# Optimization experiments

Hardware: AMD Instinct MI355X
Metric: run time of the kernel (lower is better)

## Reference

```python
import jax, jax.numpy as jnp
import numpy as np
from jax.ops import segment_sum

N_NODES = 10000
N_EDGES = 320000


def leaky_relu(x):
    return jnp.where(x >= 0, x, 0.01 * x)


def gcn_layer(edge_h, src, dst, W, b):
    # (1) node h = mean of incoming edge features
    deg = segment_sum(jnp.ones((edge_h.shape[0],), edge_h.dtype), dst, num_segments=N_NODES)
    deg = jnp.maximum(deg, 1.0)
    h = segment_sum(edge_h, dst, num_segments=N_NODES) / deg[:, None]
    # (2) update_all: node h = sum over in-edges of src node h
    h2 = segment_sum(h[src], dst, num_segments=N_NODES)
    # (3) edge h = mean of endpoint node features
    eh = 0.5 * (h2[src] + h2[dst])
    # (4) linear on edge features
    return eh @ W.T + b


def setup_inputs() -> dict:
    key = jax.random.key(0)
    ks = jax.random.split(key, 20)
    d_in, d_h, d_out = 128, 256, 64
    inp = {
        'inputs1': jax.random.normal(ks[0], (N_EDGES, d_in), jnp.float32),
        'src1': jax.random.randint(ks[1], (N_EDGES,), 0, N_NODES, jnp.int32),
        'dst1': jax.random.randint(ks[2], (N_EDGES,), 0, N_NODES, jnp.int32),
        'inputs2': jax.random.normal(ks[3], (N_EDGES, d_in), jnp.float32),
        'src2': jax.random.randint(ks[4], (N_EDGES,), 0, N_NODES, jnp.int32),
        'dst2': jax.random.randint(ks[5], (N_EDGES,), 0, N_NODES, jnp.int32),
        'W11': jax.random.normal(ks[6], (d_h, d_in), jnp.float32) * 0.05,
        'b11': jax.random.normal(ks[7], (d_h,), jnp.float32) * 0.05,
        'W12': jax.random.normal(ks[8], (d_h, d_h), jnp.float32) * 0.05,
        'b12': jax.random.normal(ks[9], (d_h,), jnp.float32) * 0.05,
        'W21': jax.random.normal(ks[10], (d_h, d_in), jnp.float32) * 0.05,
        'b21': jax.random.normal(ks[11], (d_h,), jnp.float32) * 0.05,
        'W22': jax.random.normal(ks[12], (d_h, d_h), jnp.float32) * 0.05,
        'b22': jax.random.normal(ks[13], (d_h,), jnp.float32) * 0.05,
        'W3': jax.random.normal(ks[14], (d_out, 2 * d_h), jnp.float32) * 0.05,
        'b3': jax.random.normal(ks[15], (d_out,), jnp.float32) * 0.05,
    }
    return inp


def reference(inputs1, src1, dst1, inputs2, src2, dst2,
              W11, b11, W12, b12, W21, b21, W22, b22, W3, b3):
    h1 = leaky_relu(gcn_layer(inputs1, src1, dst1, W11, b11))
    h1 = leaky_relu(gcn_layer(h1, src1, dst1, W12, b12))
    h1 = jnp.mean(h1, axis=0)
    h2 = leaky_relu(gcn_layer(inputs2, src2, dst2, W21, b21))
    h2 = leaky_relu(gcn_layer(h2, src2, dst2, W22, b22))
    h2 = jnp.mean(h2, axis=0)
    out = jnp.concatenate((h1, h2), axis=0)
    return out @ W3.T + b3
```

## Files before the change

### kernel.cpp

```cpp
#include <hip/hip_runtime.h>
#include <cstddef>

#define NN 10000

typedef unsigned int u32;
typedef unsigned short u16;
typedef __attribute__((ext_vector_type(8))) short short8;
typedef __attribute__((ext_vector_type(4))) float f32x4;

__device__ __forceinline__ float lrelu(float x) { return x >= 0.f ? x : 0.01f * x; }

__device__ __forceinline__ float bf_lo(u32 v) { union { u32 i; float f; } c; c.i = v << 16; return c.f; }
__device__ __forceinline__ float bf_hi(u32 v) { union { u32 i; float f; } c; c.i = v & 0xFFFF0000u; return c.f; }
__device__ __forceinline__ u32 rne_bits(float f) {
  union { float f; u32 i; } c; c.f = f;
  return c.i + 0x7FFFu + ((c.i >> 16) & 1u);
}
__device__ __forceinline__ u32 pack2(float a, float b) {
  return (rne_bits(a) >> 16) | (rne_bits(b) & 0xFFFF0000u);
}

__global__ __launch_bounds__(256) void wconv_kernel(
    const float* __restrict__ a, const float* __restrict__ b,
    const float* __restrict__ c, const float* __restrict__ d,
    u16* __restrict__ oa, u16* __restrict__ ob,
    u16* __restrict__ oc, u16* __restrict__ od,
    int* __restrict__ degbase ) {
  int i = blockIdx.x * 256 + threadIdx.x;
  if (i < 32768) oa[i] = (u16)(rne_bits(a[i]) >> 16);
  else if (i < 98304) ob[i - 32768] = (u16)(rne_bits(b[i - 32768]) >> 16);
  else if (i < 131072) oc[i - 98304] = (u16)(rne_bits(c[i - 98304]) >> 16);
  else if (i < 196608) od[i - 131072] = (u16)(rne_bits(d[i - 131072]) >> 16);
  if (i < 4 * NN) degbase[i] = 0;
}

__global__ __launch_bounds__(256) void count_b_kernel(const int* __restrict__ dstA,
// ... 16 lines not shown
  __shared__ int wsum[16];
  __shared__ int wpre[16];
  __shared__ int carry_s;
  const int tid = threadIdx.x;
  const int lane = tid & 63, w = tid >> 6;
  if (tid == 0) carry_s = 0;
  __syncthreads();
  for (int base = 0; base < n; base += 1024) {
    int i = base + tid;
    int x = (i < n) ? degi[i] : 0;
    int v = x;
#pragma unroll
    for (int d = 1; d < 64; d <<= 1) {
      int t = __shfl_up(v, d);
      if (lane >= d) v += t;
    }
    if (lane == 63) wsum[w] = v;
    __syncthreads();
    if (tid == 0) {
      int s = carry_s;
#pragma unroll
      for (int j = 0; j < 16; ++j) { int t = wsum[j]; wpre[j] = s; s += t; }
      carry_s = s;
    }
    __syncthreads();
    if (i < n) {
      off[i] = wpre[w] + (v - x);
      rdeg[i] = 1.0f / fmaxf((float)x, 1.0f);
    }
    __syncthreads();
  }
}

__global__ __launch_bounds__(256) void fill_b_kernel(const int* __restrict__ srcA,
                                                     const int* __restrict__ dstA,
                                                     const int* __restrict__ srcB,
                                                     const int* __restrict__ dstB,
                                                     const int* __restrict__ offbase,
                                                     int* __restrict__ degbase,
                                                     int* __restrict__ eid_sb,
                                                     int* __restrict__ esrc_sb, int E) {
  const int g = blockIdx.y;
  const int* src = g ? srcB : srcA;
  const int* dst = g ? dstB : dstA;
  const int* off = offbase + (size_t)g * NN;
  int* cursor = degbase + (size_t)g * 2 * NN + NN;
  int* eid_s = eid_sb + (size_t)g * E;
  int* esrc_s = esrc_sb + (size_t)g * E;
  int e = blockIdx.x * 256 + threadIdx.x;
  if (e < E) {
    int d = dst[e];
    int p = off[d] + atomicAdd(&cursor[d], 1);
    eid_s[p] = e;
    esrc_s[p] = src[e];
  }
}

__global__ __launch_bounds__(256) void gatherA_b_kernel(
    const float* __restrict__ featA, const float* __restrict__ featB,
    const int* __restrict__ gidxb, const int* __restrict__ offbase,
    const int* __restrict__ degbase, const float* __restrict__ rdegbase,
    u32* __restrict__ outbfb , int E) {
  const int g = blockIdx.y;
  const float* feat = g ? featB : featA;
  const int* gidx = gidxb + (size_t)g * E;
  const int* off = offbase + (size_t)g * NN;
  const int* degi = degbase + (size_t)g * 2 * NN;
  const float* rdeg = rdegbase + (size_t)g * NN;
  u32* outbf = outbfb + (size_t)g * NN * 64;
  const int n = (blockIdx.x << 2) + (threadIdx.x >> 6);
  const int lane = threadIdx.x & 63;
  const int hl = lane & 31, h = lane >> 5;
  const int o = off[n], d = degi[n];
  const int fo = hl << 2;
  float4 acc = make_float4(0.f, 0.f, 0.f, 0.f);
  for (int c0 = 0; c0 < d; c0 += 64) {
    const int m = min(64, d - c0);
    const int gg = (lane < m) ? gidx[o + c0 + lane] : 0;
    const int pairs = m >> 1;
    int i = 0;
    for (; i + 4 <= pairs; i += 4) {
      const int e0 = 2 * i + h;
      const int s0 = __shfl(gg, e0), s1 = __shfl(gg, e0 + 2);
      const int s2 = __shfl(gg, e0 + 4), s3 = __shfl(gg, e0 + 6);
      const float4 v0 = *(const float4*)&feat[(s0 << 7) + fo];
      const float4 v1 = *(const float4*)&feat[(s1 << 7) + fo];
      const float4 v2 = *(const float4*)&feat[(s2 << 7) + fo];
      const float4 v3 = *(const float4*)&feat[(s3 << 7) + fo];
      acc.x += (v0.x + v1.x) + (v2.x + v3.x);
      acc.y += (v0.y + v1.y) + (v2.y + v3.y);
      acc.z += (v0.z + v1.z) + (v2.z + v3.z);
      acc.w += (v0.w + v1.w) + (v2.w + v3.w);
    }
    for (; i < pairs; ++i) {
      const int s0 = __shfl(gg, 2 * i + h);
      const float4 v0 = *(const float4*)&feat[(s0 << 7) + fo];
      acc.x += v0.x; acc.y += v0.y; acc.z += v0.z; acc.w += v0.w;
    }
    if (m & 1) {
      const int s0 = __shfl(gg, m - 1);
      const float wgt = (h == 0) ? 1.f : 0.f;
      const float4 v0 = *(const float4*)&feat[(s0 << 7) + fo];
      acc.x = fmaf(v0.x, wgt, acc.x);
      acc.y = fmaf(v0.y, wgt, acc.y);
      acc.z = fmaf(v0.z, wgt, acc.z);
      acc.w = fmaf(v0.w, wgt, acc.w);
    }
  }
  acc.x += __shfl(acc.x, lane ^ 32);
  acc.y += __shfl(acc.y, lane ^ 32);
  acc.z += __shfl(acc.z, lane ^ 32);
  acc.w += __shfl(acc.w, lane ^ 32);
  if (h == 0) {
    const float sc = rdeg[n];
    uint2 r;
    r.x = pack2(acc.x * sc, acc.y * sc);
    r.y = pack2(acc.z * sc, acc.w * sc);
    *(uint2*)&outbf[(size_t)n * 64 + (hl << 1)] = r;
  }
}

__global__ __launch_bounds__(256) void gatherB_b_kernel(
    const u32* __restrict__ featb , const int* __restrict__ gidxb,
    const int* __restrict__ offbase, const int* __restrict__ degbase,
    u32* __restrict__ outbfb, int E) {
  const int g = blockIdx.y;
  const u32* feat = featb + (size_t)g * NN * 64;
  const int* gidx = gidxb + (size_t)g * E;
  const int* off = offbase + (size_t)g * NN;
  const int* degi = degbase + (size_t)g * 2 * NN;
  u32* outbf = outbfb + (size_t)g * NN * 64;
  const int n = (blockIdx.x << 2) + (threadIdx.x >> 6);
  const int lane = threadIdx.x & 63;
  const int hl = lane & 31, h = lane >> 5;
  const int o = off[n], d = degi[n];
  const int fo = hl << 1;
  float4 acc = make_float4(0.f, 0.f, 0.f, 0.f);
  for (int c0 = 0; c0 < d; c0 += 64) {
    const int m = min(64, d - c0);
    const int gg = (lane < m) ? gidx[o + c0 + lane] : 0;
    const int pairs = m >> 1;
    int i = 0;
    for (; i + 4 <= pairs; i += 4) {
      const int e0 = 2 * i + h;
      const int s0 = __shfl(gg, e0), s1 = __shfl(gg, e0 + 2);
      const int s2 = __shfl(gg, e0 + 4), s3 = __shfl(gg, e0 + 6);
      const uint2 v0 = *(const uint2*)&feat[(s0 << 6) + fo];
      const uint2 v1 = *(const uint2*)&feat[(s1 << 6) + fo];
      const uint2 v2 = *(const uint2*)&feat[(s2 << 6) + fo];
      const uint2 v3 = *(const uint2*)&feat[(s3 << 6) + fo];
      acc.x += (bf_lo(v0.x) + bf_lo(v1.x)) + (bf_lo(v2.x) + bf_lo(v3.x));
      acc.y += (bf_hi(v0.x) + bf_hi(v1.x)) + (bf_hi(v2.x) + bf_hi(v3.x));
      acc.z += (bf_lo(v0.y) + bf_lo(v1.y)) + (bf_lo(v2.y) + bf_lo(v3.y));
      acc.w += (bf_hi(v0.y) + bf_hi(v1.y)) + (bf_hi(v2.y) + bf_hi(v3.y));
    }
    for (; i < pairs; ++i) {
      const int s0 = __shfl(gg, 2 * i + h);
      const uint2 v0 = *(const uint2*)&feat[(s0 << 6) + fo];
      acc.x += bf_lo(v0.x); acc.y += bf_hi(v0.x);
      acc.z += bf_lo(v0.y); acc.w += bf_hi(v0.y);
    }
    if (m & 1) {
      const int s0 = __shfl(gg, m - 1);
      const float wgt = (h == 0) ? 1.f : 0.f;
      const uint2 v0 = *(const uint2*)&feat[(s0 << 6) + fo];
      acc.x = fmaf(bf_lo(v0.x), wgt, acc.x);
      acc.y = fmaf(bf_hi(v0.x), wgt, acc.y);
      acc.z = fmaf(bf_lo(v0.y), wgt, acc.z);
      acc.w = fmaf(bf_hi(v0.y), wgt, acc.w);
    }
  }
  acc.x += __shfl(acc.x, lane ^ 32);
  acc.y += __shfl(acc.y, lane ^ 32);
  acc.z += __shfl(acc.z, lane ^ 32);
  acc.w += __shfl(acc.w, lane ^ 32);
  if (h == 0) {
    uint2 r;
    r.x = pack2(acc.x, acc.y);
    r.y = pack2(acc.z, acc.w);
    *(uint2*)&outbf[(size_t)n * 64 + (hl << 1)] = r;
  }
}

__device__ __forceinline__ void acc_bf8n(float4& aL, float4& aH, uint4 v,
                                         const float4& znL, const float4& znH,
                                         const float4& bL, const float4& bH) {
  aL.x += lrelu(0.5f * (bf_lo(v.x) + znL.x) + bL.x);
  aL.y += lrelu(0.5f * (bf_hi(v.x) + znL.y) + bL.y);
  aL.z += lrelu(0.5f * (bf_lo(v.y) + znL.z) + bL.z);
  aL.w += lrelu(0.5f * (bf_hi(v.y) + znL.w) + bL.w);
  aH.x += lrelu(0.5f * (bf_lo(v.z) + znH.x) + bH.x);
  aH.y += lrelu(0.5f * (bf_hi(v.z) + znH.y) + bH.y);
  aH.z += lrelu(0.5f * (bf_lo(v.w) + znH.z) + bH.z);
  aH.w += lrelu(0.5f * (bf_hi(v.w) + znH.w) + bH.w);
}
__device__ __forceinline__ void acc_bf8w(float4& aL, float4& aH, uint4 v,
                                         const float4& znL, const float4& znH,
                                         const float4& bL, const float4& bH, float wgt) {
  aL.x += wgt * lrelu(0.5f * (bf_lo(v.x) + znL.x) + bL.x);
  aL.y += wgt * lrelu(0.5f * (bf_hi(v.x) + znL.y) + bL.y);
  aL.z += wgt * lrelu(0.5f * (bf_lo(v.y) + znL.z) + bL.z);
  aL.w += wgt * lrelu(0.5f * (bf_hi(v.y) + znL.w) + bL.w);
  aH.x += wgt * lrelu(0.5f * (bf_lo(v.z) + znH.x) + bH.x);
  aH.y += wgt * lrelu(0.5f * (bf_hi(v.z) + znH.y) + bH.y);
  aH.z += wgt * lrelu(0.5f * (bf_lo(v.w) + znH.z) + bH.z);
  aH.w += wgt * lrelu(0.5f * (bf_hi(v.w) + znH.w) + bH.w);
}

__global__ __launch_bounds__(256) void passC_b_kernel(
    const u32* __restrict__ Zb_, const int* __restrict__ esrcb,
    const int* __restrict__ offbase, const int* __restrict__ degbase,
    const float* __restrict__ rdegbase,
    const float* __restrict__ biasA, const float* __restrict__ biasB,
    u32* __restrict__ hBb, int E) {
  const int g = blockIdx.y;
  const u32* Z = Zb_ + (size_t)g * NN * 128;
  const int* esrc = esrcb + (size_t)g * E;
  const int* off = offbase + (size_t)g * NN;
  const int* degi = degbase + (size_t)g * 2 * NN;
  const float* rdeg = rdegbase + (size_t)g * NN;
  const float* bias = g ? biasB : biasA;
  u32* hB = hBb + (size_t)g * NN * 128;
  const int n = (blockIdx.x << 2) + (threadIdx.x >> 6);
  const int lane = threadIdx.x & 63;
  const int hl = lane & 31, h = lane >> 5;
  const int o = off[n], d = degi[n];
  const int fo = hl << 2;
  const uint4 znv = *(const uint4*)&Z[(n << 7) + fo];
  const float4 znL = make_float4(bf_lo(znv.x), bf_hi(znv.x), bf_lo(znv.y), bf_hi(znv.y));
  const float4 znH = make_float4(bf_lo(znv.z), bf_hi(znv.z), bf_lo(znv.w), bf_hi(znv.w));
  const float4 bL = *(const float4*)&bias[hl << 3];
  const float4 bH = *(const float4*)&bias[(hl << 3) + 4];
  float4 aL = make_float4(0.f, 0.f, 0.f, 0.f), aH = make_float4(0.f, 0.f, 0.f, 0.f);
  for (int c0 = 0; c0 < d; c0 += 64) {
    const int m = min(64, d - c0);
    const int gg = (lane < m) ? esrc[o + c0 + lane] : 0;
    const int pairs = m >> 1;
    int i = 0;
    for (; i + 4 <= pairs; i += 4) {
      const int e0 = 2 * i + h;
      const int s0 = __shfl(gg, e0), s1 = __shfl(gg, e0 + 2);
      const int s2 = __shfl(gg, e0 + 4), s3 = __shfl(gg, e0 + 6);
      const uint4 z0 = *(const uint4*)&Z[(s0 << 7) + fo];
      const uint4 z1 = *(const uint4*)&Z[(s1 << 7) + fo];
      const uint4 z2 = *(const uint4*)&Z[(s2 << 7) + fo];
      const uint4 z3 = *(const uint4*)&Z[(s3 << 7) + fo];
      acc_bf8n(aL, aH, z0, znL, znH, bL, bH);
      acc_bf8n(aL, aH, z1, znL, znH, bL, bH);
      acc_bf8n(aL, aH, z2, znL, znH, bL, bH);
      acc_bf8n(aL, aH, z3, znL, znH, bL, bH);
    }
    for (; i < pairs; ++i) {
      const int s0 = __shfl(gg, 2 * i + h);
      const uint4 z0 = *(const uint4*)&Z[(s0 << 7) + fo];
      acc_bf8n(aL, aH, z0, znL, znH, bL, bH);
    }
    if (m & 1) {
      const int s0 = __shfl(gg, m - 1);
      const float wgt = (h == 0) ? 1.f : 0.f;
      const uint4 z0 = *(const uint4*)&Z[(s0 << 7) + fo];
      acc_bf8w(aL, aH, z0, znL, znH, bL, bH, wgt);
    }
  }
  aL.x += __shfl(aL.x, lane ^ 32); aL.y += __shfl(aL.y, lane ^ 32);
  aL.z += __shfl(aL.z, lane ^ 32); aL.w += __shfl(aL.w, lane ^ 32);
  aH.x += __shfl(aH.x, lane ^ 32); aH.y += __shfl(aH.y, lane ^ 32);
  aH.z += __shfl(aH.z, lane ^ 32); aH.w += __shfl(aH.w, lane ^ 32);
  if (h == 0) {
    const float r = rdeg[n];
    uint4 outv;
    outv.x = pack2(aL.x * r, aL.y * r);
    outv.y = pack2(aL.z * r, aL.w * r);
    outv.z = pack2(aH.x * r, aH.y * r);
    outv.w = pack2(aH.z * r, aH.w * r);
    *(uint4*)&hB[(n << 7) + fo] = outv;
  }
}

__global__ __launch_bounds__(256) void gatherC_b_kernel(
    const u32* __restrict__ featb , const int* __restrict__ gidxb,
    const int* __restrict__ offbase, const int* __restrict__ degbase,
    u32* __restrict__ outbfb, int E) {
  const int g = blockIdx.y;
  const u32* feat = featb + (size_t)g * NN * 128;
  const int* gidx = gidxb + (size_t)g * E;
  const int* off = offbase + (size_t)g * NN;
  const int* degi = degbase + (size_t)g * 2 * NN;
  u32* outbf = outbfb + (size_t)g * NN * 128;
  const int n = (blockIdx.x << 2) + (threadIdx.x >> 6);
  const int lane = threadIdx.x & 63;
  const int hl = lane & 31, h = lane >> 5;
  const int o = off[n], d = degi[n];
  const int fo = hl << 2;
  float4 aL = make_float4(0.f, 0.f, 0.f, 0.f), aH = make_float4(0.f, 0.f, 0.f, 0.f);
  for (int c0 = 0; c0 < d; c0 += 64) {
    const int m = min(64, d - c0);
    const int gg = (lane < m) ? gidx[o + c0 + lane] : 0;
    const int pairs = m >> 1;
    int i = 0;
    for (; i + 4 <= pairs; i += 4) {
      const int e0 = 2 * i + h;
      const int s0 = __shfl(gg, e0), s1 = __shfl(gg, e0 + 2);
      const int s2 = __shfl(gg, e0 + 4), s3 = __shfl(gg, e0 + 6);
      const uint4 z0 = *(const uint4*)&feat[(s0 << 7) + fo];
      const uint4 z1 = *(const uint4*)&feat[(s1 << 7) + fo];
      const uint4 z2 = *(const uint4*)&feat[(s2 << 7) + fo];
      const uint4 z3 = *(const uint4*)&feat[(s3 << 7) + fo];
      aL.x += (bf_lo(z0.x) + bf_lo(z1.x)) + (bf_lo(z2.x) + bf_lo(z3.x));
      aL.y += (bf_hi(z0.x) + bf_hi(z1.x)) + (bf_hi(z2.x) + bf_hi(z3.x));
      aL.z += (bf_lo(z0.y) + bf_lo(z1.y)) + (bf_lo(z2.y) + bf_lo(z3.y));
      aL.w += (bf_hi(z0.y) + bf_hi(z1.y)) + (bf_hi(z2.y) + bf_hi(z3.y));
      aH.x += (bf_lo(z0.z) + bf_lo(z1.z)) + (bf_lo(z2.z) + bf_lo(z3.z));
      aH.y += (bf_hi(z0.z) + bf_hi(z1.z)) + (bf_hi(z2.z) + bf_hi(z3.z));
      aH.z += (bf_lo(z0.w) + bf_lo(z1.w)) + (bf_lo(z2.w) + bf_lo(z3.w));
      aH.w += (bf_hi(z0.w) + bf_hi(z1.w)) + (bf_hi(z2.w) + bf_hi(z3.w));
    }
    for (; i < pairs; ++i) {
      const int s0 = __shfl(gg, 2 * i + h);
      const uint4 z0 = *(const uint4*)&feat[(s0 << 7) + fo];
      aL.x += bf_lo(z0.x); aL.y += bf_hi(z0.x);
      aL.z += bf_lo(z0.y); aL.w += bf_hi(z0.y);
      aH.x += bf_lo(z0.z); aH.y += bf_hi(z0.z);
      aH.z += bf_lo(z0.w); aH.w += bf_hi(z0.w);
    }
    if (m & 1) {
      const int s0 = __shfl(gg, m - 1);
      const float wgt = (h == 0) ? 1.f : 0.f;
      const uint4 z0 = *(const uint4*)&feat[(s0 << 7) + fo];
      aL.x = fmaf(bf_lo(z0.x), wgt, aL.x); aL.y = fmaf(bf_hi(z0.x), wgt, aL.y);
      aL.z = fmaf(bf_lo(z0.y), wgt, aL.z); aL.w = fmaf(bf_hi(z0.y), wgt, aL.w);
      aH.x = fmaf(bf_lo(z0.z), wgt, aH.x); aH.y = fmaf(bf_hi(z0.z), wgt, aH.y);
      aH.z = fmaf(bf_lo(z0.w), wgt, aH.z); aH.w = fmaf(bf_hi(z0.w), wgt, aH.w);
    }
  }
  aL.x += __shfl(aL.x, lane ^ 32); aL.y += __shfl(aL.y, lane ^ 32);
  aL.z += __shfl(aL.z, lane ^ 32); aL.w += __shfl(aL.w, lane ^ 32);
  aH.x += __shfl(aH.x, lane ^ 32); aH.y += __shfl(aH.y, lane ^ 32);
  aH.z += __shfl(aH.z, lane ^ 32); aH.w += __shfl(aH.w, lane ^ 32);
  if (h == 0) {
    uint4 outv;
    outv.x = pack2(aL.x, aL.y);
    outv.y = pack2(aL.z, aL.w);
    outv.z = pack2(aH.x, aH.y);
    outv.w = pack2(aH.z, aH.w);
    *(uint4*)&outbf[(n << 7) + fo] = outv;
  }
}

__global__ __launch_bounds__(256) void passE_b_kernel(
    const u32* __restrict__ Z2b, const int* __restrict__ esrcb,
    const int* __restrict__ offbase, const int* __restrict__ degbase,
    const float* __restrict__ biasA, const float* __restrict__ biasB,
    float* __restrict__ partialsb , int nNodes, int E) {
  const int g = blockIdx.y;
  const u32* Z2 = Z2b + (size_t)g * NN * 128;
  const int* esrc = esrcb + (size_t)g * E;
  const int* off = offbase + (size_t)g * NN;
  const int* degi = degbase + (size_t)g * 2 * NN;
  const float* bias = g ? biasB : biasA;
  float* partials = partialsb + (size_t)g * 256 * 256;
  const int lane = threadIdx.x & 63, w = threadIdx.x >> 6;
  const int hl = lane & 31, h = lane >> 5;
  const int gw = blockIdx.x * 4 + w, nw = gridDim.x * 4;
  const int fo = hl << 2;
  const float4 bL = *(const float4*)&bias[hl << 3];
  const float4 bH = *(const float4*)&bias[(hl << 3) + 4];
  float4 aL = make_float4(0.f, 0.f, 0.f, 0.f), aH = make_float4(0.f, 0.f, 0.f, 0.f);
  for (int n = gw; n < nNodes; n += nw) {
    const int o = off[n], d = degi[n];
    const uint4 znv = *(const uint4*)&Z2[(n << 7) + fo];
    const float4 znL = make_float4(bf_lo(znv.x), bf_hi(znv.x), bf_lo(znv.y), bf_hi(znv.y));
    const float4 znH = make_float4(bf_lo(znv.z), bf_hi(znv.z), bf_lo(znv.w), bf_hi(znv.w));
    for (int c0 = 0; c0 < d; c0 += 64) {
      const int m = min(64, d - c0);
      const int gg = (lane < m) ? esrc[o + c0 + lane] : 0;
      const int pairs = m >> 1;
      int i = 0;
      for (; i + 4 <= pairs; i += 4) {
        const int e0 = 2 * i + h;
        const int s0 = __shfl(gg, e0), s1 = __shfl(gg, e0 + 2);
        const int s2 = __shfl(gg, e0 + 4), s3 = __shfl(gg, e0 + 6);
        const uint4 z0 = *(const uint4*)&Z2[(s0 << 7) + fo];
        const uint4 z1 = *(const uint4*)&Z2[(s1 << 7) + fo];
        const uint4 z2 = *(const uint4*)&Z2[(s2 << 7) + fo];
        const uint4 z3 = *(const uint4*)&Z2[(s3 << 7) + fo];
        acc_bf8n(aL, aH, z0, znL, znH, bL, bH);
        acc_bf8n(aL, aH, z1, znL, znH, bL, bH);
        acc_bf8n(aL, aH, z2, znL, znH, bL, bH);
        acc_bf8n(aL, aH, z3, znL, znH, bL, bH);
      }
      for (; i < pairs; ++i) {
        const int s0 = __shfl(gg, 2 * i + h);
        const uint4 z0 = *(const uint4*)&Z2[(s0 << 7) + fo];
        acc_bf8n(aL, aH, z0, znL, znH, bL, bH);
      }
      if (m & 1) {
        const int s0 = __shfl(gg, m - 1);
        const float wgt = (h == 0) ? 1.f : 0.f;
        const uint4 z0 = *(const uint4*)&Z2[(s0 << 7) + fo];
        acc_bf8w(aL, aH, z0, znL, znH, bL, bH, wgt);
      }
    }
  }
  aL.x += __shfl(aL.x, lane ^ 32); aL.y += __shfl(aL.y, lane ^ 32);
  aL.z += __shfl(aL.z, lane ^ 32); aL.w += __shfl(aL.w, lane ^ 32);
  aH.x += __shfl(aH.x, lane ^ 32); aH.y += __shfl(aH.y, lane ^ 32);
  aH.z += __shfl(aH.z, lane ^ 32); aH.w += __shfl(aH.w, lane ^ 32);
  __shared__ float red[4][256];
  if (h == 0) {
    *(float4*)&red[w][hl << 3] = aL;
    *(float4*)&red[w][(hl << 3) + 4] = aH;
  }
  __syncthreads();
  if (w == 0) {
    float4 s0 = *(const float4*)&red[0][lane << 2];
    float4 s1 = *(const float4*)&red[1][lane << 2];
    float4 s2 = *(const float4*)&red[2][lane << 2];
    float4 s3 = *(const float4*)&red[3][lane << 2];
    float4 s = make_float4(s0.x + s1.x + s2.x + s3.x, s0.y + s1.y + s2.y + s3.y,
                           s0.z + s1.z + s2.z + s3.z, s0.w + s1.w + s2.w + s3.w);
    *(float4*)&partials[(size_t)blockIdx.x * 256 + (lane << 2)] = s;
  }
}

__global__ __launch_bounds__(1024) void final_fused_kernel(
    const float* __restrict__ partialsb ,
    const float* __restrict__ W3, const float* __restrict__ b3,
    float* __restrict__ out, float invE) {
  __shared__ float smacc[512];
  __shared__ float red[16][64];
  const int tid = threadIdx.x;
  {
    const int half = tid >> 9;
    const int gk = tid & 511;
    const float* P = partialsb + (size_t)gk;
    const int g = gk >> 8, k = gk & 255;
    const float* base = partialsb + (size_t)g * 256 * 256 + k;
    float s = 0.f;
    for (int b = half * 128; b < half * 128 + 128; ++b) s += base[(size_t)b * 256];
    (void)P;
    __shared__ float tmp[2][512];
    tmp[half][gk] = s;
    __syncthreads();
    if (half == 0) smacc[gk] = tmp[0][gk] + tmp[1][gk];
  }
  __syncthreads();
  const int j = tid & 63, part = tid >> 6;
  float acc = 0.f;
  for (int kk = 0; kk < 32; ++kk) {
    const int k = part * 32 + kk;
    acc += smacc[k] * W3[(size_t)j * 512 + k];
  }
  red[part][j] = acc;
  __syncthreads();
  if (part == 0) {
    float s = 0.f;
#pragma unroll
    for (int p = 0; p < 16; ++p) s += red[p][j];
    out[j] = b3[j] + s * invE;
  }
}

template <int K>
__global__ __launch_bounds__(256) void gemm_mfma_b_kernel(const u16* __restrict__ Ab,
                                                          const u16* __restrict__ WA,
                                                          const u16* __restrict__ WB,
                                                          u16* __restrict__ Cb, int N) {
  const int g = blockIdx.z;
  const u16* A = Ab + (size_t)g * NN * K;
  const u16* Wb = g ? WB : WA;
  u16* C = Cb + (size_t)g * NN * 256;
  const int lane = threadIdx.x & 63;
  const int w = threadIdx.x >> 6;
  const int wm = w >> 1, wn = w & 1;
  const int bn = blockIdx.x * 64 + wm * 32;
  const int bo = blockIdx.y * 64 + wn * 32;
  const int r0 = lane & 15;
  const int kq = lane >> 4;
// ... 33 lines not shown

extern "C" void kernel_launch(void* const* d_in, const int* in_sizes, int n_in,
                              void* d_out, int out_size, void* d_ws, size_t ws_size,
                              hipStream_t stream) {
  const float* in1 = (const float*)d_in[0];
  const int* src1 = (const int*)d_in[1];
  const int* dst1 = (const int*)d_in[2];
  const float* in2 = (const float*)d_in[3];
  const int* src2 = (const int*)d_in[4];
  const int* dst2 = (const int*)d_in[5];
  const float* W11 = (const float*)d_in[6];
  const float* b11 = (const float*)d_in[7];
  const float* W12 = (const float*)d_in[8];
  const float* b12 = (const float*)d_in[9];
  const float* W21 = (const float*)d_in[10];
  const float* b21 = (const float*)d_in[11];
  const float* W22 = (const float*)d_in[12];
  const float* b22 = (const float*)d_in[13];
  const float* W3 = (const float*)d_in[14];
  const float* b3 = (const float*)d_in[15];
  const int E = in_sizes[1];
  const int N = NN;

  char* base = (char*)d_ws;
  size_t pos = 0;
  auto carve = [&](size_t bytes) -> char* {
    char* p = base + pos;
    pos = (pos + bytes + 511) & ~(size_t)511;
    return p;
  };
  int* degbase = (int*)carve((size_t)2 * 2 * N * sizeof(int));
  int* offb = (int*)carve((size_t)2 * N * sizeof(int));
  float* rdegb = (float*)carve((size_t)2 * N * sizeof(float));
  int* eid_sb = (int*)carve((size_t)2 * E * sizeof(int));
  int* esrc_sb = (int*)carve((size_t)2 * E * sizeof(int));
  u32* Hb = (u32*)carve((size_t)2 * N * 64 * sizeof(u32));
  u32* H2b = (u32*)carve((size_t)2 * N * 64 * sizeof(u32));
  u32* Zb = (u32*)carve((size_t)2 * N * 128 * sizeof(u32));
  u32* HBb = (u32*)carve((size_t)2 * N * 128 * sizeof(u32));
  u32* H2Bb = (u32*)carve((size_t)2 * N * 128 * sizeof(u32));
  u16* Wa1 = (u16*)carve((size_t)32768 * sizeof(u16));
  u16* Wb1 = (u16*)carve((size_t)65536 * sizeof(u16));
  u16* Wa2 = (u16*)carve((size_t)32768 * sizeof(u16));
  u16* Wb2 = (u16*)carve((size_t)65536 * sizeof(u16));
  float* partialsb = (float*)carve((size_t)2 * 256 * 256 * sizeof(float));
  (void)ws_size; (void)n_in; (void)out_size;

  const int EB = (E + 255) / 256;
  const int NB = N / 4;
  const dim3 g2(EB, 2);
  const dim3 n2(NB, 2);
  const dim3 gemm_grid((N + 63) / 64, 4, 2);

  wconv_kernel<<<768, 256, 0, stream>>>(W11, W12, W21, W22, Wa1, Wb1, Wa2, Wb2, degbase);

  count_b_kernel<<<g2, 256, 0, stream>>>(dst1, dst2, degbase, E);
  scan_b_kernel<<<2, 1024, 0, stream>>>(degbase, offb, rdegb, N);
  fill_b_kernel<<<g2, 256, 0, stream>>>(src1, dst1, src2, dst2, offb, degbase, eid_sb, esrc_sb, E);

  gatherA_b_kernel<<<n2, 256, 0, stream>>>(in1, in2, eid_sb, offb, degbase, rdegb, Hb, E);
  gatherB_b_kernel<<<n2, 256, 0, stream>>>(Hb, esrc_sb, offb, degbase, H2b, E);
  gemm_mfma_b_kernel<128><<<gemm_grid, 256, 0, stream>>>((const u16*)H2b, Wa1, Wa2, (u16*)Zb, N);

  passC_b_kernel<<<n2, 256, 0, stream>>>(Zb, esrc_sb, offb, degbase, rdegb, b11, b21, HBb, E);
  gatherC_b_kernel<<<n2, 256, 0, stream>>>(HBb, esrc_sb, offb, degbase, H2Bb, E);
  gemm_mfma_b_kernel<256><<<gemm_grid, 256, 0, stream>>>((const u16*)H2Bb, Wb1, Wb2, (u16*)Zb, N);

  passE_b_kernel<<<dim3(256, 2), 256, 0, stream>>>(Zb, esrc_sb, offb, degbase, b12, b22,
                                                   partialsb, N, E);
  final_fused_kernel<<<1, 1024, 0, stream>>>(partialsb, W3, b3, (float*)d_out, 1.0f / (float)E);
}
```

Before: 345.2 us.

## Scatter edge features into dst-sorted bf16 buffer, split feature halves across blocks

```diff
diff --git a/kernel.cpp b/kernel.cpp
--- a/kernel.cpp
+++ b/kernel.cpp
@@ -2,6 +2,7 @@
 #include <cstddef>
 
 #define NN 10000
+#define NB 2500
 
 typedef unsigned int u32;
 typedef unsigned short u16;
@@ -84,38 +85,44 @@
   }
 }
 
-__global__ __launch_bounds__(256) void fill_b_kernel(const int* __restrict__ srcA,
-                                                     const int* __restrict__ dstA,
-                                                     const int* __restrict__ srcB,
-                                                     const int* __restrict__ dstB,
-                                                     const int* __restrict__ offbase,
-                                                     int* __restrict__ degbase,
-                                                     int* __restrict__ eid_sb,
-                                                     int* __restrict__ esrc_sb, int E) {
+__global__ __launch_bounds__(256) void scatterA_b_kernel(
+    const float* __restrict__ featA, const float* __restrict__ featB,
+    const int* __restrict__ srcA, const int* __restrict__ dstA,
+    const int* __restrict__ srcB, const int* __restrict__ dstB,
+    const int* __restrict__ offbase, int* __restrict__ degbase,
+    u32* __restrict__ tmpb , int* __restrict__ esrc_sb, int E) {
   const int g = blockIdx.y;
+  const float* feat = g ? featB : featA;
   const int* src = g ? srcB : srcA;
   const int* dst = g ? dstB : dstA;
   const int* off = offbase + (size_t)g * NN;
   int* cursor = degbase + (size_t)g * 2 * NN + NN;
-  int* eid_s = eid_sb + (size_t)g * E;
+  u32* tmp = tmpb + (size_t)g * E * 64;
   int* esrc_s = esrc_sb + (size_t)g * E;
-  int e = blockIdx.x * 256 + threadIdx.x;
-  if (e < E) {
-    int d = dst[e];
-    int p = off[d] + atomicAdd(&cursor[d], 1);
-    eid_s[p] = e;
-    esrc_s[p] = src[e];
-  }
-}
-
-__global__ __launch_bounds__(256) void gatherA_b_kernel(
-    const float* __restrict__ featA, const float* __restrict__ featB,
-    const int* __restrict__ gidxb, const int* __restrict__ offbase,
+  const int idx = blockIdx.x * 8 + (threadIdx.x >> 5);
+  const int lane32 = threadIdx.x & 31;
+  if (idx >= E) return;
+  int p0 = 0, sv = 0;
+  if (lane32 == 0) {
+    const int dv = dst[idx];
+    sv = src[idx];
+    p0 = off[dv] + atomicAdd(&cursor[dv], 1);
+  }
+  const int p = __shfl(p0, threadIdx.x & 32);
+  const float4 v = *(const float4*)&feat[(size_t)idx * 128 + (lane32 << 2)];
+  uint2 o;
+  o.x = pack2(v.x, v.y);
+  o.y = pack2(v.z, v.w);
+  *(uint2*)&tmp[(size_t)p * 64 + (lane32 << 1)] = o;
+  if (lane32 == 0) esrc_s[p] = sv;
+}
+
+__global__ __launch_bounds__(256) void reduceA_b_kernel(
+    const u32* __restrict__ tmpb, const int* __restrict__ offbase,
     const int* __restrict__ degbase, const float* __restrict__ rdegbase,
     u32* __restrict__ outbfb , int E) {
   const int g = blockIdx.y;
-  const float* feat = g ? featB : featA;
-  const int* gidx = gidxb + (size_t)g * E;
+  const u32* tmp = tmpb + (size_t)g * E * 64;
   const int* off = offbase + (size_t)g * NN;
   const int* degi = degbase + (size_t)g * 2 * NN;
   const float* rdeg = rdegbase + (size_t)g * NN;
@@ -124,40 +131,23 @@
   const int lane = threadIdx.x & 63;
   const int hl = lane & 31, h = lane >> 5;
   const int o = off[n], d = degi[n];
-  const int fo = hl << 2;
+  const u32* basep = tmp + (size_t)o * 64 + (hl << 1);
   float4 acc = make_float4(0.f, 0.f, 0.f, 0.f);
-  for (int c0 = 0; c0 < d; c0 += 64) {
-    const int m = min(64, d - c0);
-    const int gg = (lane < m) ? gidx[o + c0 + lane] : 0;
-    const int pairs = m >> 1;
-    int i = 0;
-    for (; i + 4 <= pairs; i += 4) {
-      const int e0 = 2 * i + h;
-      const int s0 = __shfl(gg, e0), s1 = __shfl(gg, e0 + 2);
-      const int s2 = __shfl(gg, e0 + 4), s3 = __shfl(gg, e0 + 6);
-      const float4 v0 = *(const float4*)&feat[(s0 << 7) + fo];
-      const float4 v1 = *(const float4*)&feat[(s1 << 7) + fo];
-      const float4 v2 = *(const float4*)&feat[(s2 << 7) + fo];
-      const float4 v3 = *(const float4*)&feat[(s3 << 7) + fo];
-      acc.x += (v0.x + v1.x) + (v2.x + v3.x);
-      acc.y += (v0.y + v1.y) + (v2.y + v3.y);
-      acc.z += (v0.z + v1.z) + (v2.z + v3.z);
-      acc.w += (v0.w + v1.w) + (v2.w + v3.w);
-    }
-    for (; i < pairs; ++i) {
-      const int s0 = __shfl(gg, 2 * i + h);
-      const float4 v0 = *(const float4*)&feat[(s0 << 7) + fo];
-      acc.x += v0.x; acc.y += v0.y; acc.z += v0.z; acc.w += v0.w;
-    }
-    if (m & 1) {
-      const int s0 = __shfl(gg, m - 1);
-      const float wgt = (h == 0) ? 1.f : 0.f;
-      const float4 v0 = *(const float4*)&feat[(s0 << 7) + fo];
-      acc.x = fmaf(v0.x, wgt, acc.x);
-      acc.y = fmaf(v0.y, wgt, acc.y);
-      acc.z = fmaf(v0.z, wgt, acc.z);
-      acc.w = fmaf(v0.w, wgt, acc.w);
-    }
+  int j = h;
+  for (; j + 6 < d; j += 8) {
+    const uint2 v0 = *(const uint2*)(basep + (size_t)j * 64);
+    const uint2 v1 = *(const uint2*)(basep + (size_t)(j + 2) * 64);
+    const uint2 v2 = *(const uint2*)(basep + (size_t)(j + 4) * 64);
+    const uint2 v3 = *(const uint2*)(basep + (size_t)(j + 6) * 64);
+    acc.x += (bf_lo(v0.x) + bf_lo(v1.x)) + (bf_lo(v2.x) + bf_lo(v3.x));
+    acc.y += (bf_hi(v0.x) + bf_hi(v1.x)) + (bf_hi(v2.x) + bf_hi(v3.x));
+    acc.z += (bf_lo(v0.y) + bf_lo(v1.y)) + (bf_lo(v2.y) + bf_lo(v3.y));
+    acc.w += (bf_hi(v0.y) + bf_hi(v1.y)) + (bf_hi(v2.y) + bf_hi(v3.y));
+  }
+  for (; j < d; j += 2) {
+    const uint2 v0 = *(const uint2*)(basep + (size_t)j * 64);
+    acc.x += bf_lo(v0.x); acc.y += bf_hi(v0.x);
+    acc.z += bf_lo(v0.y); acc.w += bf_hi(v0.y);
   }
   acc.x += __shfl(acc.x, lane ^ 32);
   acc.y += __shfl(acc.y, lane ^ 32);
@@ -176,13 +166,16 @@
     const u32* __restrict__ featb , const int* __restrict__ gidxb,
     const int* __restrict__ offbase, const int* __restrict__ degbase,
     u32* __restrict__ outbfb, int E) {
-  const int g = blockIdx.y;
+  const int bid = blockIdx.x;
+  const int r = bid & 7, t = bid >> 3;
+  const int g = r >> 2;
+  const int nb = t * 4 + (r & 3);
   const u32* feat = featb + (size_t)g * NN * 64;
   const int* gidx = gidxb + (size_t)g * E;
   const int* off = offbase + (size_t)g * NN;
   const int* degi = degbase + (size_t)g * 2 * NN;
   u32* outbf = outbfb + (size_t)g * NN * 64;
-  const int n = (blockIdx.x << 2) + (threadIdx.x >> 6);
+  const int n = (nb << 2) + (threadIdx.x >> 6);
   const int lane = threadIdx.x & 63;
   const int hl = lane & 31, h = lane >> 5;
   const int o = off[n], d = degi[n];
@@ -227,36 +220,18 @@
   acc.z += __shfl(acc.z, lane ^ 32);
   acc.w += __shfl(acc.w, lane ^ 32);
   if (h == 0) {
-    uint2 r;
-    r.x = pack2(acc.x, acc.y);
-    r.y = pack2(acc.z, acc.w);
-    *(uint2*)&outbf[(size_t)n * 64 + (hl << 1)] = r;
-  }
-}
-
-__device__ __forceinline__ void acc_bf8n(float4& aL, float4& aH, uint4 v,
-                                         const float4& znL, const float4& znH,
-                                         const float4& bL, const float4& bH) {
-  aL.x += lrelu(0.5f * (bf_lo(v.x) + znL.x) + bL.x);
-  aL.y += lrelu(0.5f * (bf_hi(v.x) + znL.y) + bL.y);
-  aL.z += lrelu(0.5f * (bf_lo(v.y) + znL.z) + bL.z);
-  aL.w += lrelu(0.5f * (bf_hi(v.y) + znL.w) + bL.w);
-  aH.x += lrelu(0.5f * (bf_lo(v.z) + znH.x) + bH.x);
-  aH.y += lrelu(0.5f * (bf_hi(v.z) + znH.y) + bH.y);
-  aH.z += lrelu(0.5f * (bf_lo(v.w) + znH.z) + bH.z);
-  aH.w += lrelu(0.5f * (bf_hi(v.w) + znH.w) + bH.w);
-}
-__device__ __forceinline__ void acc_bf8w(float4& aL, float4& aH, uint4 v,
-                                         const float4& znL, const float4& znH,
-                                         const float4& bL, const float4& bH, float wgt) {
-  aL.x += wgt * lrelu(0.5f * (bf_lo(v.x) + znL.x) + bL.x);
-  aL.y += wgt * lrelu(0.5f * (bf_hi(v.x) + znL.y) + bL.y);
-  aL.z += wgt * lrelu(0.5f * (bf_lo(v.y) + znL.z) + bL.z);
-  aL.w += wgt * lrelu(0.5f * (bf_hi(v.y) + znL.w) + bL.w);
-  aH.x += wgt * lrelu(0.5f * (bf_lo(v.z) + znH.x) + bH.x);
-  aH.y += wgt * lrelu(0.5f * (bf_hi(v.z) + znH.y) + bH.y);
-  aH.z += wgt * lrelu(0.5f * (bf_lo(v.w) + znH.z) + bH.z);
-  aH.w += wgt * lrelu(0.5f * (bf_hi(v.w) + znH.w) + bH.w);
+    uint2 r2;
+    r2.x = pack2(acc.x, acc.y);
+    r2.y = pack2(acc.z, acc.w);
+    *(uint2*)&outbf[(size_t)n * 64 + (hl << 1)] = r2;
+  }
+}
+
+__device__ __forceinline__ void acc_bf4(float4& a, uint2 v, const float4& zn, const float4& bb) {
+  a.x += lrelu(0.5f * (bf_lo(v.x) + zn.x) + bb.x);
+  a.y += lrelu(0.5f * (bf_hi(v.x) + zn.y) + bb.y);
+  a.z += lrelu(0.5f * (bf_lo(v.y) + zn.z) + bb.z);
+  a.w += lrelu(0.5f * (bf_hi(v.y) + zn.w) + bb.w);
 }
 
 __global__ __launch_bounds__(256) void passC_b_kernel(
@@ -265,7 +240,10 @@
     const float* __restrict__ rdegbase,
     const float* __restrict__ biasA, const float* __restrict__ biasB,
     u32* __restrict__ hBb, int E) {
-  const int g = blockIdx.y;
+  const int bid = blockIdx.x;
+  const int r = bid & 7, t = bid >> 3;
+  const int g = r >> 2, fh = (r >> 1) & 1;
+  const int nb = t * 2 + (r & 1);
   const u32* Z = Zb_ + (size_t)g * NN * 128;
   const int* esrc = esrcb + (size_t)g * E;
   const int* off = offbase + (size_t)g * NN;
@@ -273,17 +251,15 @@
   const float* rdeg = rdegbase + (size_t)g * NN;
   const float* bias = g ? biasB : biasA;
   u32* hB = hBb + (size_t)g * NN * 128;
-  const int n = (blockIdx.x << 2) + (threadIdx.x >> 6);
+  const int n = (nb << 2) + (threadIdx.x >> 6);
   const int lane = threadIdx.x & 63;
   const int hl = lane & 31, h = lane >> 5;
   const int o = off[n], d = degi[n];
-  const int fo = hl << 2;
-  const uint4 znv = *(const uint4*)&Z[(n << 7) + fo];
-  const float4 znL = make_float4(bf_lo(znv.x), bf_hi(znv.x), bf_lo(znv.y), bf_hi(znv.y));
-  const float4 znH = make_float4(bf_lo(znv.z), bf_hi(znv.z), bf_lo(znv.w), bf_hi(znv.w));
-  const float4 bL = *(const float4*)&bias[hl << 3];
-  const float4 bH = *(const float4*)&bias[(hl << 3) + 4];
-  float4 aL = make_float4(0.f, 0.f, 0.f, 0.f), aH = make_float4(0.f, 0.f, 0.f, 0.f);
+  const int fo = (fh << 6) + (hl << 1);
+  const uint2 znv = *(const uint2*)&Z[(n << 7) + fo];
+  const float4 zn = make_float4(bf_lo(znv.x), bf_hi(znv.x), bf_lo(znv.y), bf_hi(znv.y));
+  const float4 bb = *(const float4*)&bias[(fh << 7) + (hl << 2)];
+  float4 a = make_float4(0.f, 0.f, 0.f, 0.f);
   for (int c0 = 0; c0 < d; c0 += 64) {
     const int m = min(64, d - c0);
     const int gg = (lane < m) ? esrc[o + c0 + lane] : 0;
@@ -293,39 +269,34 @@
       const int e0 = 2 * i + h;
       const int s0 = __shfl(gg, e0), s1 = __shfl(gg, e0 + 2);
       const int s2 = __shfl(gg, e0 + 4), s3 = __shfl(gg, e0 + 6);
-      const uint4 z0 = *(const uint4*)&Z[(s0 << 7) + fo];
-      const uint4 z1 = *(const uint4*)&Z[(s1 << 7) + fo];
-      const uint4 z2 = *(const uint4*)&Z[(s2 << 7) + fo];
-      const uint4 z3 = *(const uint4*)&Z[(s3 << 7) + fo];
-      acc_bf8n(aL, aH, z0, znL, znH, bL, bH);
-      acc_bf8n(aL, aH, z1, znL, znH, bL, bH);
-      acc_bf8n(aL, aH, z2, znL, znH, bL, bH);
-      acc_bf8n(aL, aH, z3, znL, znH, bL, bH);
+      const uint2 z0 = *(const uint2*)&Z[(s0 << 7) + fo];
+      const uint2 z1 = *(const uint2*)&Z[(s1 << 7) + fo];
+      const uint2 z2 = *(const uint2*)&Z[(s2 << 7) + fo];
+      const uint2 z3 = *(const uint2*)&Z[(s3 << 7) + fo];
+      acc_bf4(a, z0, zn, bb);
+      acc_bf4(a, z1, zn, bb);
+      acc_bf4(a, z2, zn, bb);
+      acc_bf4(a, z3, zn, bb);
     }
     for (; i < pairs; ++i) {
       const int s0 = __shfl(gg, 2 * i + h);
-      const uint4 z0 = *(const uint4*)&Z[(s0 << 7) + fo];
-      acc_bf8n(aL, aH, z0, znL, znH, bL, bH);
+      const uint2 z0 = *(const uint2*)&Z[(s0 << 7) + fo];
+      acc_bf4(a, z0, zn, bb);
     }
     if (m & 1) {
       const int s0 = __shfl(gg, m - 1);
-      const float wgt = (h == 0) ? 1.f : 0.f;
-      const uint4 z0 = *(const uint4*)&Z[(s0 << 7) + fo];
-      acc_bf8w(aL, aH, z0, znL, znH, bL, bH, wgt);
-    }
-  }
-  aL.x += __shfl(aL.x, lane ^ 32); aL.y += __shfl(aL.y, lane ^ 32);
-  aL.z += __shfl(aL.z, lane ^ 32); aL.w += __shfl(aL.w, lane ^ 32);
-  aH.x += __shfl(aH.x, lane ^ 32); aH.y += __shfl(aH.y, lane ^ 32);
-  aH.z += __shfl(aH.z, lane ^ 32); aH.w += __shfl(aH.w, lane ^ 32);
+      const uint2 z0 = *(const uint2*)&Z[(s0 << 7) + fo];
+      if (h == 0) acc_bf4(a, z0, zn, bb);
+    }
+  }
+  a.x += __shfl(a.x, lane ^ 32); a.y += __shfl(a.y, lane ^ 32);
+  a.z += __shfl(a.z, lane ^ 32); a.w += __shfl(a.w, lane ^ 32);
   if (h == 0) {
-    const float r = rdeg[n];
-    uint4 outv;
-    outv.x = pack2(aL.x * r, aL.y * r);
-    outv.y = pack2(aL.z * r, aL.w * r);
-    outv.z = pack2(aH.x * r, aH.y * r);
-    outv.w = pack2(aH.z * r, aH.w * r);
-    *(uint4*)&hB[(n << 7) + fo] = outv;
+    const float rr = rdeg[n];
+    uint2 outv;
+    outv.x = pack2(a.x * rr, a.y * rr);
+    outv.y = pack2(a.z * rr, a.w * rr);
+    *(uint2*)&hB[(n << 7) + fo] = outv;
   }
 }
 
@@ -333,18 +304,21 @@
     const u32* __restrict__ featb , const int* __restrict__ gidxb,
     const int* __restrict__ offbase, const int* __restrict__ degbase,
     u32* __restrict__ outbfb, int E) {
-  const int g = blockIdx.y;
+  const int bid = blockIdx.x;
+  const int r = bid & 7, t = bid >> 3;
+  const int g = r >> 2, fh = (r >> 1) & 1;
+  const int nb = t * 2 + (r & 1);
   const u32* feat = featb + (size_t)g * NN * 128;
   const int* gidx = gidxb + (size_t)g * E;
   const int* off = offbase + (size_t)g * NN;
   const int* degi = degbase + (size_t)g * 2 * NN;
   u32* outbf = outbfb + (size_t)g * NN * 128;
-  const int n = (blockIdx.x << 2) + (threadIdx.x >> 6);
+  const int n = (nb << 2) + (threadIdx.x >> 6);
   const int lane = threadIdx.x & 63;
   const int hl = lane & 31, h = lane >> 5;
   const int o = off[n], d = degi[n];
-  const int fo = hl << 2;
-  float4 aL = make_float4(0.f, 0.f, 0.f, 0.f), aH = make_float4(0.f, 0.f, 0.f, 0.f);
+  const int fo = (fh << 6) + (hl << 1);
+  float4 a = make_float4(0.f, 0.f, 0.f, 0.f);
   for (int c0 = 0; c0 < d; c0 += 64) {
     const int m = min(64, d - c0);
     const int gg = (lane < m) ? gidx[o + c0 + lane] : 0;
@@ -354,48 +328,37 @@
       const int e0 = 2 * i + h;
       const int s0 = __shfl(gg, e0), s1 = __shfl(gg, e0 + 2);
       const int s2 = __shfl(gg, e0 + 4), s3 = __shfl(gg, e0 + 6);
-      const uint4 z0 = *(const uint4*)&feat[(s0 << 7) + fo];
-      const uint4 z1 = *(const uint4*)&feat[(s1 << 7) + fo];
-      const uint4 z2 = *(const uint4*)&feat[(s2 << 7) + fo];
-      const uint4 z3 = *(const uint4*)&feat[(s3 << 7) + fo];
-      aL.x += (bf_lo(z0.x) + bf_lo(z1.x)) + (bf_lo(z2.x) + bf_lo(z3.x));
-      aL.y += (bf_hi(z0.x) + bf_hi(z1.x)) + (bf_hi(z2.x) + bf_hi(z3.x));
-      aL.z += (bf_lo(z0.y) + bf_lo(z1.y)) + (bf_lo(z2.y) + bf_lo(z3.y));
-      aL.w += (bf_hi(z0.y) + bf_hi(z1.y)) + (bf_hi(z2.y) + bf_hi(z3.y));
-      aH.x += (bf_lo(z0.z) + bf_lo(z1.z)) + (bf_lo(z2.z) + bf_lo(z3.z));
-      aH.y += (bf_hi(z0.z) + bf_hi(z1.z)) + (bf_hi(z2.z) + bf_hi(z3.z));
-      aH.z += (bf_lo(z0.w) + bf_lo(z1.w)) + (bf_lo(z2.w) + bf_lo(z3.w));
-      aH.w += (bf_hi(z0.w) + bf_hi(z1.w)) + (bf_hi(z2.w) + bf_hi(z3.w));
+      const uint2 z0 = *(const uint2*)&feat[(s0 << 7) + fo];
+      const uint2 z1 = *(const uint2*)&feat[(s1 << 7) + fo];
+      const uint2 z2 = *(const uint2*)&feat[(s2 << 7) + fo];
+      const uint2 z3 = *(const uint2*)&feat[(s3 << 7) + fo];
+      a.x += (bf_lo(z0.x) + bf_lo(z1.x)) + (bf_lo(z2.x) + bf_lo(z3.x));
+      a.y += (bf_hi(z0.x) + bf_hi(z1.x)) + (bf_hi(z2.x) + bf_hi(z3.x));
+      a.z += (bf_lo(z0.y) + bf_lo(z1.y)) + (bf_lo(z2.y) + bf_lo(z3.y));
+      a.w += (bf_hi(z0.y) + bf_hi(z1.y)) + (bf_hi(z2.y) + bf_hi(z3.y));
     }
     for (; i < pairs; ++i) {
       const int s0 = __shfl(gg, 2 * i + h);
-      const uint4 z0 = *(const uint4*)&feat[(s0 << 7) + fo];
-      aL.x += bf_lo(z0.x); aL.y += bf_hi(z0.x);
-      aL.z += bf_lo(z0.y); aL.w += bf_hi(z0.y);
-      aH.x += bf_lo(z0.z); aH.y += bf_hi(z0.z);
-      aH.z += bf_lo(z0.w); aH.w += bf_hi(z0.w);
+      const uint2 z0 = *(const uint2*)&feat[(s0 << 7) + fo];
+      a.x += bf_lo(z0.x); a.y += bf_hi(z0.x);
+      a.z += bf_lo(z0.y); a.w += bf_hi(z0.y);
     }
     if (m & 1) {
       const int s0 = __shfl(gg, m - 1);
-      const float wgt = (h == 0) ? 1.f : 0.f;
-      const uint4 z0 = *(const uint4*)&feat[(s0 << 7) + fo];
-      aL.x = fmaf(bf_lo(z0.x), wgt, aL.x); aL.y = fmaf(bf_hi(z0.x), wgt, aL.y);
-      aL.z = fmaf(bf_lo(z0.y), wgt, aL.z); aL.w = fmaf(bf_hi(z0.y), wgt, aL.w);
-      aH.x = fmaf(bf_lo(z0.z), wgt, aH.x); aH.y = fmaf(bf_hi(z0.z), wgt, aH.y);
-      aH.z = fmaf(bf_lo(z0.w), wgt, aH.z); aH.w = fmaf(bf_hi(z0.w), wgt, aH.w);
-    }
-  }
-  aL.x += __shfl(aL.x, lane ^ 32); aL.y += __shfl(aL.y, lane ^ 32);
-  aL.z += __shfl(aL.z, lane ^ 32); aL.w += __shfl(aL.w, lane ^ 32);
-  aH.x += __shfl(aH.x, lane ^ 32); aH.y += __shfl(aH.y, lane ^ 32);
-  aH.z += __shfl(aH.z, lane ^ 32); aH.w += __shfl(aH.w, lane ^ 32);
+      const uint2 z0 = *(const uint2*)&feat[(s0 << 7) + fo];
+      if (h == 0) {
+        a.x += bf_lo(z0.x); a.y += bf_hi(z0.x);
+        a.z += bf_lo(z0.y); a.w += bf_hi(z0.y);
+      }
+    }
+  }
+  a.x += __shfl(a.x, lane ^ 32); a.y += __shfl(a.y, lane ^ 32);
+  a.z += __shfl(a.z, lane ^ 32); a.w += __shfl(a.w, lane ^ 32);
   if (h == 0) {
-    uint4 outv;
-    outv.x = pack2(aL.x, aL.y);
-    outv.y = pack2(aL.z, aL.w);
-    outv.z = pack2(aH.x, aH.y);
-    outv.w = pack2(aH.z, aH.w);
-    *(uint4*)&outbf[(n << 7) + fo] = outv;
+    uint2 outv;
+    outv.x = pack2(a.x, a.y);
+    outv.y = pack2(a.z, a.w);
+    *(uint2*)&outbf[(n << 7) + fo] = outv;
   }
 }
 
@@ -404,25 +367,25 @@
     const int* __restrict__ offbase, const int* __restrict__ degbase,
     const float* __restrict__ biasA, const float* __restrict__ biasB,
     float* __restrict__ partialsb , int nNodes, int E) {
-  const int g = blockIdx.y;
+  const int bid = blockIdx.x;
+  const int r = bid & 7, t = bid >> 3;
+  const int g = r >> 2, fh = (r >> 1) & 1;
+  const int blk = t * 2 + (r & 1);
   const u32* Z2 = Z2b + (size_t)g * NN * 128;
   const int* esrc = esrcb + (size_t)g * E;
   const int* off = offbase + (size_t)g * NN;
   const int* degi = degbase + (size_t)g * 2 * NN;
   const float* bias = g ? biasB : biasA;
-  float* partials = partialsb + (size_t)g * 256 * 256;
+  float* partials = partialsb + (size_t)((g * 2 + fh) * 128 + blk) * 128;
   const int lane = threadIdx.x & 63, w = threadIdx.x >> 6;
   const int hl = lane & 31, h = lane >> 5;
-  const int gw = blockIdx.x * 4 + w, nw = gridDim.x * 4;
-  const int fo = hl << 2;
-  const float4 bL = *(const float4*)&bias[hl << 3];
-  const float4 bH = *(const float4*)&bias[(hl << 3) + 4];
-  float4 aL = make_float4(0.f, 0.f, 0.f, 0.f), aH = make_float4(0.f, 0.f, 0.f, 0.f);
-  for (int n = gw; n < nNodes; n += nw) {
+  const int fo = (fh << 6) + (hl << 1);
+  const float4 bb = *(const float4*)&bias[(fh << 7) + (hl << 2)];
+  float4 a = make_float4(0.f, 0.f, 0.f, 0.f);
+  for (int n = blk * 4 + w; n < nNodes; n += 512) {
     const int o = off[n], d = degi[n];
-    const uint4 znv = *(const uint4*)&Z2[(n << 7) + fo];
-    const float4 znL = make_float4(bf_lo(znv.x), bf_hi(znv.x), bf_lo(znv.y), bf_hi(znv.y));
-    const float4 znH = make_float4(bf_lo(znv.z), bf_hi(znv.z), bf_lo(znv.w), bf_hi(znv.w));
+    const uint2 znv = *(const uint2*)&Z2[(n << 7) + fo];
+    const float4 zn = make_float4(bf_lo(znv.x), bf_hi(znv.x), bf_lo(znv.y), bf_hi(znv.y));
     for (int c0 = 0; c0 < d; c0 += 64) {
       const int m = min(64, d - c0);
       const int gg = (lane < m) ? esrc[o + c0 + lane] : 0;
@@ -432,47 +395,34 @@
         const int e0 = 2 * i + h;
         const int s0 = __shfl(gg, e0), s1 = __shfl(gg, e0 + 2);
         const int s2 = __shfl(gg, e0 + 4), s3 = __shfl(gg, e0 + 6);
-        const uint4 z0 = *(const uint4*)&Z2[(s0 << 7) + fo];
-        const uint4 z1 = *(const uint4*)&Z2[(s1 << 7) + fo];
-        const uint4 z2 = *(const uint4*)&Z2[(s2 << 7) + fo];
-        const uint4 z3 = *(const uint4*)&Z2[(s3 << 7) + fo];
-        acc_bf8n(aL, aH, z0, znL, znH, bL, bH);
-        acc_bf8n(aL, aH, z1, znL, znH, bL, bH);
-        acc_bf8n(aL, aH, z2, znL, znH, bL, bH);
-        acc_bf8n(aL, aH, z3, znL, znH, bL, bH);
+        const uint2 z0 = *(const uint2*)&Z2[(s0 << 7) + fo];
+        const uint2 z1 = *(const uint2*)&Z2[(s1 << 7) + fo];
+        const uint2 z2 = *(const uint2*)&Z2[(s2 << 7) + fo];
+        const uint2 z3 = *(const uint2*)&Z2[(s3 << 7) + fo];
+        acc_bf4(a, z0, zn, bb);
+        acc_bf4(a, z1, zn, bb);
+        acc_bf4(a, z2, zn, bb);
+        acc_bf4(a, z3, zn, bb);
       }
       for (; i < pairs; ++i) {
         const int s0 = __shfl(gg, 2 * i + h);
-        const uint4 z0 = *(const uint4*)&Z2[(s0 << 7) + fo];
-        acc_bf8n(aL, aH, z0, znL, znH, bL, bH);
+        const uint2 z0 = *(const uint2*)&Z2[(s0 << 7) + fo];
+        acc_bf4(a, z0, zn, bb);
       }
       if (m & 1) {
         const int s0 = __shfl(gg, m - 1);
-        const float wgt = (h == 0) ? 1.f : 0.f;
-        const uint4 z0 = *(const uint4*)&Z2[(s0 << 7) + fo];
-        acc_bf8w(aL, aH, z0, znL, znH, bL, bH, wgt);
+        const uint2 z0 = *(const uint2*)&Z2[(s0 << 7) + fo];
+        if (h == 0) acc_bf4(a, z0, zn, bb);
       }
     }
   }
-  aL.x += __shfl(aL.x, lane ^ 32); aL.y += __shfl(aL.y, lane ^ 32);
-  aL.z += __shfl(aL.z, lane ^ 32); aL.w += __shfl(aL.w, lane ^ 32);
-  aH.x += __shfl(aH.x, lane ^ 32); aH.y += __shfl(aH.y, lane ^ 32);
-  aH.z += __shfl(aH.z, lane ^ 32); aH.w += __shfl(aH.w, lane ^ 32);
-  __shared__ float red[4][256];
-  if (h == 0) {
-    *(float4*)&red[w][hl << 3] = aL;
-    *(float4*)&red[w][(hl << 3) + 4] = aH;
-  }
+  a.x += __shfl(a.x, lane ^ 32); a.y += __shfl(a.y, lane ^ 32);
+  a.z += __shfl(a.z, lane ^ 32); a.w += __shfl(a.w, lane ^ 32);
+  __shared__ float red[4][128];
+  if (h == 0) *(float4*)&red[w][hl << 2] = a;
   __syncthreads();
-  if (w == 0) {
-    float4 s0 = *(const float4*)&red[0][lane << 2];
-    float4 s1 = *(const float4*)&red[1][lane << 2];
-    float4 s2 = *(const float4*)&red[2][lane << 2];
-    float4 s3 = *(const float4*)&red[3][lane << 2];
-    float4 s = make_float4(s0.x + s1.x + s2.x + s3.x, s0.y + s1.y + s2.y + s3.y,
-                           s0.z + s1.z + s2.z + s3.z, s0.w + s1.w + s2.w + s3.w);
-    *(float4*)&partials[(size_t)blockIdx.x * 256 + (lane << 2)] = s;
-  }
+  const int tid = threadIdx.x;
+  if (tid < 128) partials[tid] = red[0][tid] + red[1][tid] + red[2][tid] + red[3][tid];
 }
 
 __global__ __launch_bounds__(1024) void final_fused_kernel(
@@ -480,22 +430,19 @@
     const float* __restrict__ W3, const float* __restrict__ b3,
     float* __restrict__ out, float invE) {
   __shared__ float smacc[512];
+  __shared__ float tmp2[2][512];
   __shared__ float red[16][64];
   const int tid = threadIdx.x;
   {
     const int half = tid >> 9;
-    const int gk = tid & 511;
-    const float* P = partialsb + (size_t)gk;
-    const int g = gk >> 8, k = gk & 255;
-    const float* base = partialsb + (size_t)g * 256 * 256 + k;
+    const int q = tid & 511;
+    const float* basep = partialsb + (size_t)(q >> 7) * 128 * 128 + (q & 127);
     float s = 0.f;
-    for (int b = half * 128; b < half * 128 + 128; ++b) s += base[(size_t)b * 256];
-    (void)P;
-    __shared__ float tmp[2][512];
-    tmp[half][gk] = s;
-    __syncthreads();
-    if (half == 0) smacc[gk] = tmp[0][gk] + tmp[1][gk];
-  }
+    for (int b = half * 64; b < half * 64 + 64; ++b) s += basep[(size_t)b * 128];
+    tmp2[half][q] = s;
+  }
+  __syncthreads();
+  if (tid < 512) smacc[tid] = tmp2[0][tid] + tmp2[1][tid];
   __syncthreads();
   const int j = tid & 63, part = tid >> 6;
   float acc = 0.f;
@@ -595,8 +542,8 @@
   int* degbase = (int*)carve((size_t)2 * 2 * N * sizeof(int));
   int* offb = (int*)carve((size_t)2 * N * sizeof(int));
   float* rdegb = (float*)carve((size_t)2 * N * sizeof(float));
-  int* eid_sb = (int*)carve((size_t)2 * E * sizeof(int));
   int* esrc_sb = (int*)carve((size_t)2 * E * sizeof(int));
+  u32* tmpb = (u32*)carve((size_t)2 * E * 64 * sizeof(u32));
   u32* Hb = (u32*)carve((size_t)2 * N * 64 * sizeof(u32));
   u32* H2b = (u32*)carve((size_t)2 * N * 64 * sizeof(u32));
   u32* Zb = (u32*)carve((size_t)2 * N * 128 * sizeof(u32));
@@ -606,30 +553,29 @@
   u16* Wb1 = (u16*)carve((size_t)65536 * sizeof(u16));
   u16* Wa2 = (u16*)carve((size_t)32768 * sizeof(u16));
   u16* Wb2 = (u16*)carve((size_t)65536 * sizeof(u16));
-  float* partialsb = (float*)carve((size_t)2 * 256 * 256 * sizeof(float));
+  float* partialsb = (float*)carve((size_t)2 * 2 * 128 * 128 * sizeof(float));
   (void)ws_size; (void)n_in; (void)out_size;
 
   const int EB = (E + 255) / 256;
-  const int NB = N / 4;
   const dim3 g2(EB, 2);
-  const dim3 n2(NB, 2);
   const dim3 gemm_grid((N + 63) / 64, 4, 2);
 
   wconv_kernel<<<768, 256, 0, stream>>>(W11, W12, W21, W22, Wa1, Wb1, Wa2, Wb2, degbase);
 
   count_b_kernel<<<g2, 256, 0, stream>>>(dst1, dst2, degbase, E);
   scan_b_kernel<<<2, 1024, 0, stream>>>(degbase, offb, rdegb, N);
-  fill_b_kernel<<<g2, 256, 0, stream>>>(src1, dst1, src2, dst2, offb, degbase, eid_sb, esrc_sb, E);
-
-  gatherA_b_kernel<<<n2, 256, 0, stream>>>(in1, in2, eid_sb, offb, degbase, rdegb, Hb, E);
-  gatherB_b_kernel<<<n2, 256, 0, stream>>>(Hb, esrc_sb, offb, degbase, H2b, E);
+
+  scatterA_b_kernel<<<dim3((E + 7) / 8, 2), 256, 0, stream>>>(
+      in1, in2, src1, dst1, src2, dst2, offb, degbase, tmpb, esrc_sb, E);
+  reduceA_b_kernel<<<dim3(NB, 2), 256, 0, stream>>>(tmpb, offb, degbase, rdegb, Hb, E);
+
+  gatherB_b_kernel<<<2 * NB, 256, 0, stream>>>(Hb, esrc_sb, offb, degbase, H2b, E);
   gemm_mfma_b_kernel<128><<<gemm_grid, 256, 0, stream>>>((const u16*)H2b, Wa1, Wa2, (u16*)Zb, N);
 
-  passC_b_kernel<<<n2, 256, 0, stream>>>(Zb, esrc_sb, offb, degbase, rdegb, b11, b21, HBb, E);
-  gatherC_b_kernel<<<n2, 256, 0, stream>>>(HBb, esrc_sb, offb, degbase, H2Bb, E);
+  passC_b_kernel<<<4 * NB, 256, 0, stream>>>(Zb, esrc_sb, offb, degbase, rdegb, b11, b21, HBb, E);
+  gatherC_b_kernel<<<4 * NB, 256, 0, stream>>>(HBb, esrc_sb, offb, degbase, H2Bb, E);
   gemm_mfma_b_kernel<256><<<gemm_grid, 256, 0, stream>>>((const u16*)H2Bb, Wb1, Wb2, (u16*)Zb, N);
 
-  passE_b_kernel<<<dim3(256, 2), 256, 0, stream>>>(Zb, esrc_sb, offb, degbase, b12, b22,
-                                                   partialsb, N, E);
+  passE_b_kernel<<<512, 256, 0, stream>>>(Zb, esrc_sb, offb, degbase, b12, b22, partialsb, N, E);
   final_fused_kernel<<<1, 1024, 0, stream>>>(partialsb, W3, b3, (float*)d_out, 1.0f / (float)E);
 }
```

Measured after the change: 395.3 us. 1.15x slower.
